# Performance work log

Hardware: AMD Instinct MI355X
Metric: run time of the kernel (lower is better)

The kernel has to match this reference:

```python
import jax, jax.numpy as jnp
import numpy as np

D_MODEL = 1024
NUM_HEADS = 16
HEAD_DIM = D_MODEL // NUM_HEADS
B, S = 4, 2048


def _xavier(key, shape, gain=0.1):
    fan_in, fan_out = shape[1], shape[0]
    a = gain * np.sqrt(6.0 / (fan_in + fan_out))
    return jax.random.uniform(key, shape, jnp.float32, -a, a)


def setup_inputs() -> dict:
    key = jax.random.key(0)
    ks = jax.random.split(key, 11)
    inp = {
        "q": jax.random.normal(ks[0], (B, S, D_MODEL), jnp.float32),
        "k": jax.random.normal(ks[1], (B, S, D_MODEL), jnp.float32),
        "v": jax.random.normal(ks[2], (B, S, D_MODEL), jnp.float32),
        # nn.Linear weights are [out, in]; y = x @ W.T + b
        "Wq": _xavier(ks[3], (D_MODEL, D_MODEL)),
        "bq": jnp.zeros((D_MODEL,), jnp.float32),
        "Wk": _xavier(ks[4], (D_MODEL, D_MODEL)),
        "bk": jnp.zeros((D_MODEL,), jnp.float32),
        "Wv": _xavier(ks[5], (D_MODEL, D_MODEL)),
        "bv": jnp.zeros((D_MODEL,), jnp.float32),
        "Wo": _xavier(ks[6], (D_MODEL, D_MODEL)),
        "bo": jnp.zeros((D_MODEL,), jnp.float32),
    }
    return inp


def reference(q, k, v, Wq, bq, Wk, bk, Wv, bv, Wo, bo):
    b = q.shape[0]
    qh = (q @ Wq.T + bq).reshape(b, -1, NUM_HEADS, HEAD_DIM).transpose(0, 2, 1, 3)
    kh = (k @ Wk.T + bk).reshape(b, -1, NUM_HEADS, HEAD_DIM).transpose(0, 2, 1, 3)
    vh = (v @ Wv.T + bv).reshape(b, -1, NUM_HEADS, HEAD_DIM).transpose(0, 2, 1, 3)
    # NOTE: original (buggy) module scales by sqrt(d_model), not sqrt(head_dim)
    scale = 1.0 / jnp.sqrt(jnp.float32(D_MODEL))
    scores = jnp.einsum('bhqd,bhkd->bhqk', qh, kh) * scale  # [B,H,S,S]
    attn = jax.nn.softmax(scores, axis=-1)
    out = jnp.einsum('bhqk,bhkd->bhqd', attn, vh)
    out = out.transpose(0, 2, 1, 3).reshape(b, -1, D_MODEL)
    return out @ Wo.T + bo
```

## Files before the change

### kernel.cpp

```cpp
#include <hip/hip_runtime.h>

typedef unsigned short u16;
typedef short bf16x8 __attribute__((ext_vector_type(8)));
typedef float f32x4 __attribute__((ext_vector_type(4)));
typedef u16 u16x8 __attribute__((ext_vector_type(8)));

__device__ __forceinline__ u16 f2bf(float f) {
  unsigned u = __float_as_uint(f);
  u = u + 0x7fffu + ((u >> 16) & 1u);
  return (u16)(u >> 16);
}

__device__ __forceinline__ float fexp2(float x) {
#if __has_builtin(__builtin_amdgcn_exp2f)
  return __builtin_amdgcn_exp2f(x);
#else
  return exp2f(x);
#endif
}

#define GLD16(ldsp, gp)                                                         \
  __builtin_amdgcn_global_load_lds(                                             \
      (__attribute__((address_space(1))) void*)(void*)(gp),                     \
      (__attribute__((address_space(3))) void*)(ldsp), 16, 0, 0)

#define CVTPK(dst, lo, hi)                                                      \
  asm("v_cvt_pk_bf16_f32 %0, %1, %2" : "=v"(dst) : "v"(lo), "v"(hi))
#define PACK8(dst, a0, a1, a2, a3, a4, a5, a6, a7)                              \
  do {                                                                          \
    union { unsigned u_[4]; bf16x8 v_; } c_;                                    \
    CVTPK(c_.u_[0], a0, a1); CVTPK(c_.u_[1], a2, a3);                           \
    CVTPK(c_.u_[2], a4, a5); CVTPK(c_.u_[3], a6, a7);                           \
    dst = c_.v_;                                                                \
  } while (0)

__global__ __launch_bounds__(256) void pack_w4(const float* __restrict__ w0,
                                               const float* __restrict__ w1,
                                               const float* __restrict__ w2,
                                               const float* __restrict__ w3,
                                               u16* __restrict__ out) {
  int i = blockIdx.x * 256 + threadIdx.x;
  int which = i >> 17;
  const float* src = which == 0 ? w0 : which == 1 ? w1 : which == 2 ? w2 : w3;
  int j = i & 131071;
  const float4* p = (const float4*)src + (size_t)j * 2;
  float4 a = p[0], b = p[1];
  u16x8 r;
  r[0] = f2bf(a.x); r[1] = f2bf(a.y); r[2] = f2bf(a.z); r[3] = f2bf(a.w);
  r[4] = f2bf(b.x); r[5] = f2bf(b.y); r[6] = f2bf(b.z); r[7] = f2bf(b.w);
  *(u16x8*)(out + (size_t)i * 8) = r;
}

__global__ __launch_bounds__(256, 4)
void gemm_qkv(const float* __restrict__ qi, const float* __restrict__ ki,
              const float* __restrict__ vi, const u16* __restrict__ wbf,
              const float* __restrict__ bq, const float* __restrict__ bk,
              const float* __restrict__ bv, u16* __restrict__ qo,
              u16* __restrict__ ko, u16* __restrict__ vo) {
  constexpr int K = 1024;
  __shared__ __align__(16) u16 As[128 * 64];
  __shared__ __align__(16) u16 Bs[128 * 64];
  const int z = blockIdx.z;
  const float* Af = z == 0 ? qi : z == 1 ? ki : vi;
  const u16* Bw = wbf + ((size_t)z << 20);
  const float* bias = z == 0 ? bq : z == 1 ? bk : bv;

  const int t = threadIdx.x;
  const int w = t >> 6, l = t & 63;
  const int lr = l & 15, lg = l >> 4;
  const int flat = blockIdx.x | (blockIdx.y << 3);
  const int swz = ((flat & 7) << 6) | (flat >> 3);
  const int row0 = (swz >> 3) * 128, col0 = (swz & 7) * 128;
  const int wm = (w >> 1) * 64, wn = (w & 1) * 64;

  f32x4 acc[4][4] = {};

  const int ar = t >> 3;
  const int xw = ((t & 7) ^ (ar & 7)) * 16;
  const float* gA = Af + (size_t)(row0 + ar) * K + (t & 7) * 8;
  const u16* gB = Bw + (size_t)(col0 + ar) * K + (((t & 7) ^ (ar & 7)) * 8);
  u16* lB = &Bs[w * 512];

  float4 a0[4], a1[4];
#pragma unroll
  for (int j = 0; j < 4; ++j) {
    const float* p = gA + (size_t)j * 32 * K;
    a0[j] = *(const float4*)p;
    a1[j] = *(const float4*)(p + 4);
  }

  for (int kt = 0; kt < 16; ++kt) {
#pragma unroll
    for (int j = 0; j < 4; ++j)
      GLD16(lB + j * 2048, gB + (size_t)j * 32 * K + kt * 64);
#pragma unroll
    for (int j = 0; j < 4; ++j) {
      bf16x8 c;
      PACK8(c, a0[j].x, a0[j].y, a0[j].z, a0[j].w, a1[j].x, a1[j].y, a1[j].z, a1[j].w);
      *(bf16x8*)((char*)As + (ar + j * 32) * 128 + xw) = c;
    }
    __syncthreads();
    if (kt < 15) {
#pragma unroll
      for (int j = 0; j < 4; ++j) {
        const float* p = gA + (size_t)j * 32 * K + (kt + 1) * 64;
        a0[j] = *(const float4*)p;
        a1[j] = *(const float4*)(p + 4);
      }
    }
#pragma unroll
    for (int kh2 = 0; kh2 < 2; ++kh2) {
      bf16x8 aF[4], bF[4];
      const int bc = (kh2 * 64 + lg * 16) ^ ((lr & 7) * 16);
#pragma unroll
      for (int mi = 0; mi < 4; ++mi)
        aF[mi] = *(const bf16x8*)((const char*)As + (wm + mi * 16 + lr) * 128 + bc);
#pragma unroll
      for (int ni = 0; ni < 4; ++ni)
        bF[ni] = *(const bf16x8*)((const char*)Bs + (wn + ni * 16 + lr) * 128 + bc);
#pragma unroll
      for (int mi = 0; mi < 4; ++mi)
#pragma unroll
        for (int ni = 0; ni < 4; ++ni)
          acc[mi][ni] = __builtin_amdgcn_mfma_f32_16x16x32_bf16(aF[mi], bF[ni],
                                                                acc[mi][ni], 0, 0, 0);
    }
    __syncthreads();
  }

#pragma unroll
  for (int mi = 0; mi < 4; ++mi) {
#pragma unroll
    for (int ni = 0; ni < 4; ++ni) {
      const int n = col0 + wn + ni * 16 + lr;
      const float bvv = bias[n];
#pragma unroll
      for (int r = 0; r < 4; ++r) {
        const int m = row0 + wm + mi * 16 + lg * 4 + r;
        const float vv = acc[mi][ni][r] + bvv;
        const int bI = m >> 11, s = m & 2047, h = n >> 6, d = n & 63;
        if (z == 0) {
          qo[((size_t)((bI << 4) + h) * 2048 + s) * 64 + d] = f2bf(vv * 0.045084223f);
        } else if (z == 1) {
          ko[((size_t)((bI << 4) + h) * 2048 + s) * 64 + d] = f2bf(vv);
        } else {
          int bh = (bI << 4) + h, tile = s >> 6, kp = s & 63;
          int kM = kp >> 5, k5 = kp & 31;
          int kpp = kM * 32 + ((k5 >> 2) & 3) * 8 + (k5 >> 4) * 4 + (k5 & 3);
          int chunk = (kpp >> 3) ^ (d & 7);
          vo[((size_t)bh << 17) + tile * 4096 + d * 64 + chunk * 8 + (kpp & 7)] = f2bf(vv);
        }
      }
    }
  }
}

__global__ __launch_bounds__(256, 3)
void gemm_out(const u16* __restrict__ A, const u16* __restrict__ B,
              const float* __restrict__ bias, float* __restrict__ outp) {
  constexpr int K = 1024;
  __shared__ __align__(16) u16 As[128 * 64];
  __shared__ __align__(16) u16 Bs[128 * 64];
  const int t = threadIdx.x;
  const int w = t >> 6;
  const int l = t & 63;
  const int lr = l & 15, lg = l >> 4;
  const int flat = blockIdx.x | (blockIdx.y << 3);
  const int swz = ((flat & 7) << 6) | (flat >> 3);
  const int row0 = (swz >> 3) * 128, col0 = (swz & 7) * 128;
  const int wm = (w >> 1) * 64, wn = (w & 1) * 64;

  f32x4 acc[4][4] = {};

  const int srow = t >> 3;
  const int scol = ((t & 7) ^ (srow & 7)) * 8;
  const u16* gA = A + (size_t)(row0 + srow) * K + scol;
  const u16* gB = B + (size_t)(col0 + srow) * K + scol;
  u16* lA = &As[w * 512];
  u16* lB = &Bs[w * 512];

  for (int k0 = 0; k0 < K; k0 += 64) {
#pragma unroll
    for (int j = 0; j < 4; ++j) {
      GLD16(lA + j * 2048, gA + (size_t)j * 32 * K + k0);
      GLD16(lB + j * 2048, gB + (size_t)j * 32 * K + k0);
    }
    __syncthreads();
#pragma unroll
    for (int kh2 = 0; kh2 < 2; ++kh2) {
      bf16x8 aF[4], bF[4];
      const int bc = (kh2 * 64 + lg * 16) ^ ((lr & 7) * 16);
#pragma unroll
      for (int mi = 0; mi < 4; ++mi)
        aF[mi] = *(const bf16x8*)((const char*)As + (wm + mi * 16 + lr) * 128 + bc);
#pragma unroll
      for (int ni = 0; ni < 4; ++ni)
        bF[ni] = *(const bf16x8*)((const char*)Bs + (wn + ni * 16 + lr) * 128 + bc);
#pragma unroll
      for (int mi = 0; mi < 4; ++mi)
#pragma unroll
        for (int ni = 0; ni < 4; ++ni)
          acc[mi][ni] = __builtin_amdgcn_mfma_f32_16x16x32_bf16(aF[mi], bF[ni],
                                                                acc[mi][ni], 0, 0, 0);
    }
    __syncthreads();
  }

#pragma unroll
  for (int mi = 0; mi < 4; ++mi)
#pragma unroll
    for (int ni = 0; ni < 4; ++ni) {
      const int n = col0 + wn + ni * 16 + lr;
      const float bv = bias[n];
#pragma unroll
      for (int r = 0; r < 4; ++r) {
        const int m = row0 + wm + mi * 16 + lg * 4 + r;
        outp[(size_t)m * 1024 + n] = acc[mi][ni][r] + bv;
      }
    }
}

__global__ __launch_bounds__(256, 4)
void attn_fwd(const u16* __restrict__ qh, const u16* __restrict__ kh,
              const u16* __restrict__ vp, u16* __restrict__ aout) {
  __shared__ __align__(16) u16 Ks[2][4096];
  __shared__ __align__(16) u16 Vl[2][4096];
  const int t = threadIdx.x;
  const int w = t >> 6, l = t & 63;
  const int lr = l & 15, lg = l >> 4;
  const int flat = blockIdx.x | (blockIdx.y << 4);
  const int swz = ((flat & 7) << 7) | (flat >> 3);
  const int qb = swz & 15, bh = swz >> 4;
  const int q0 = qb * 128 + w * 32;

  bf16x8 qf[2][2];
#pragma unroll
  for (int qi = 0; qi < 2; ++qi) {
    const u16* qp = qh + ((size_t)bh * 2048 + q0 + qi * 16 + lr) * 64 + lg * 8;
    qf[qi][0] = *(const bf16x8*)qp;
    qf[qi][1] = *(const bf16x8*)(qp + 32);
  }

  f32x4 o0[4] = {}, o1[4] = {};
  f32x4 sm0 = {}, sm1 = {};
  const bf16x8 ones = {16256, 16256, 16256, 16256, 16256, 16256, 16256, 16256};

  const int krow = t >> 3, kseg = t & 7;
  const u16* gK = kh + ((size_t)bh * 2048 + krow) * 64 + ((kseg ^ (krow & 7)) * 8);
  const u16* gV = vp + ((size_t)bh << 17) + t * 8;

  const int xo0 = (lg * 16) ^ ((lr & 7) * 16);
  const int xo1 = xo0 ^ 64;

  {
    u16* kd = &Ks[0][0] + w * 512;
    u16* vd = &Vl[0][0] + w * 512;
    GLD16(kd, gK); GLD16(kd + 2048, gK + 2048);
    GLD16(vd, gV); GLD16(vd + 2048, gV + 2048);
    gK += 4096; gV += 4096;
  }
  __syncthreads();

  for (int tix = 0; tix < 32; ++tix) {
    const int cur = tix & 1;
    if (tix < 31) {
      u16* kd = &Ks[cur ^ 1][0] + w * 512;
      u16* vd = &Vl[cur ^ 1][0] + w * 512;
      GLD16(kd, gK); GLD16(kd + 2048, gK + 2048);
      GLD16(vd, gV); GLD16(vd + 2048, gV + 2048);
      gK += 4096; gV += 4096;
    }
    const char* kb = (const char*)&Ks[cur][0];
    f32x4 s0[4], s1[4];
    __builtin_amdgcn_s_setprio(1);
#pragma unroll
    for (int cq = 0; cq < 4; ++cq) {
      const char* rowp = kb + (cq * 16 + lr) * 128;
      bf16x8 kf0 = *(const bf16x8*)(rowp + xo0);
      bf16x8 kf1 = *(const bf16x8*)(rowp + xo1);
      f32x4 a = {}, b2 = {};
      a  = __builtin_amdgcn_mfma_f32_16x16x32_bf16(kf0, qf[0][0], a, 0, 0, 0);
      a  = __builtin_amdgcn_mfma_f32_16x16x32_bf16(kf1, qf[0][1], a, 0, 0, 0);
      b2 = __builtin_amdgcn_mfma_f32_16x16x32_bf16(kf0, qf[1][0], b2, 0, 0, 0);
      b2 = __builtin_amdgcn_mfma_f32_16x16x32_bf16(kf1, qf[1][1], b2, 0, 0, 0);
      s0[cq] = a; s1[cq] = b2;
    }
    __builtin_amdgcn_s_setprio(0);
    float p0[16], p1[16];
#pragma unroll
    for (int cq = 0; cq < 4; ++cq)
#pragma unroll
      for (int r = 0; r < 4; ++r) {
        p0[cq * 4 + r] = fexp2(s0[cq][r]);
        p1[cq * 4 + r] = fexp2(s1[cq][r]);
      }
    bf16x8 pA0, pA1, pB0, pB1;
    PACK8(pA0, p0[0], p0[1], p0[2], p0[3], p0[4], p0[5], p0[6], p0[7]);
    PACK8(pA1, p0[8], p0[9], p0[10], p0[11], p0[12], p0[13], p0[14], p0[15]);
    PACK8(pB0, p1[0], p1[1], p1[2], p1[3], p1[4], p1[5], p1[6], p1[7]);
    PACK8(pB1, p1[8], p1[9], p1[10], p1[11], p1[12], p1[13], p1[14], p1[15]);
    __builtin_amdgcn_s_setprio(1);
    sm0 = __builtin_amdgcn_mfma_f32_16x16x32_bf16(pA0, ones, sm0, 0, 0, 0);
    sm0 = __builtin_amdgcn_mfma_f32_16x16x32_bf16(pA1, ones, sm0, 0, 0, 0);
    sm1 = __builtin_amdgcn_mfma_f32_16x16x32_bf16(pB0, ones, sm1, 0, 0, 0);
    sm1 = __builtin_amdgcn_mfma_f32_16x16x32_bf16(pB1, ones, sm1, 0, 0, 0);
    const char* vbb = (const char*)&Vl[cur][0];
#pragma unroll
    for (int dc = 0; dc < 4; ++dc) {
      const char* rp = vbb + (dc * 16 + lr) * 128;
      bf16x8 vA = *(const bf16x8*)(rp + xo0);
      bf16x8 vB = *(const bf16x8*)(rp + xo1);
      o0[dc] = __builtin_amdgcn_mfma_f32_16x16x32_bf16(pA0, vA, o0[dc], 0, 0, 0);
      o0[dc] = __builtin_amdgcn_mfma_f32_16x16x32_bf16(pA1, vB, o0[dc], 0, 0, 0);
      o1[dc] = __builtin_amdgcn_mfma_f32_16x16x32_bf16(pB0, vA, o1[dc], 0, 0, 0);
      o1[dc] = __builtin_amdgcn_mfma_f32_16x16x32_bf16(pB1, vB, o1[dc], 0, 0, 0);
    }
    __builtin_amdgcn_s_setprio(0);
    __syncthreads();
  }

  const int b = bh >> 4, h = bh & 15;
#pragma unroll
  for (int r = 0; r < 4; ++r) {
    const float dA = 1.f / sm0[r];
    const float dB = 1.f / sm1[r];
    const size_t rowA = (size_t)b * 2048 + q0 + lg * 4 + r;
#pragma unroll
    for (int dc = 0; dc < 4; ++dc) {
      aout[rowA * 1024 + h * 64 + dc * 16 + lr] = f2bf(o0[dc][r] * dA);
      aout[(rowA + 16) * 1024 + h * 64 + dc * 16 + lr] = f2bf(o1[dc][r] * dB);
    }
  }
}

extern "C" void kernel_launch(void* const* d_in, const int* in_sizes, int n_in,
                              void* d_out, int out_size, void* d_ws, size_t ws_size,
                              hipStream_t stream) {
  const float* q  = (const float*)d_in[0];
  const float* k  = (const float*)d_in[1];
  const float* v  = (const float*)d_in[2];
  const float* Wq = (const float*)d_in[3];
  const float* bq = (const float*)d_in[4];
  const float* Wk = (const float*)d_in[5];
  const float* bk = (const float*)d_in[6];
  const float* Wv = (const float*)d_in[7];
  const float* bv = (const float*)d_in[8];
  const float* Wo = (const float*)d_in[9];
  const float* bo = (const float*)d_in[10];

  char* ws = (char*)d_ws;
  u16* wbf  = (u16*)(ws);
  u16* aout = (u16*)(ws + (8ull << 20));
  u16* qhB  = (u16*)(ws + (24ull << 20));
  u16* khB  = (u16*)(ws + (40ull << 20));
  u16* vtB  = (u16*)(ws + (56ull << 20));

  pack_w4<<<2048, 256, 0, stream>>>(Wq, Wk, Wv, Wo, wbf);
  gemm_qkv<<<dim3(8, 64, 3), 256, 0, stream>>>(q, k, v, wbf, bq, bk, bv,
                                               qhB, khB, vtB);
  attn_fwd<<<dim3(16, 64), 256, 0, stream>>>(qhB, khB, vtB, aout);
  gemm_out<<<dim3(8, 64), 256, 0, stream>>>(aout, wbf + (3u << 20), bo,
                                            (float*)d_out);

  (void)in_sizes; (void)n_in; (void)out_size; (void)ws_size;
}
```

Before: 167.6 us.

## Software-pipeline QK^T one tile ahead of softmax/PV with triple-buffered V

Restructures the attention main loop so that the QK^T MFMAs for the next K tile are issued before the exp/pack/PV work of the current tile. V gets a three-slot ring buffer so V can be staged further ahead, and the loop is unrolled by two with alternating score registers. The goal is to overlap the exp (VALU/transcendental) work with matrix-core work and hide LDS latency. In exchange it uses more LDS and more registers, and launch bounds drop from 4 to 3 blocks per CU, which lowers occupancy.

New measurement: 172.7 us. 1.03x slower.

```diff
diff --git a/kernel.cpp b/kernel.cpp
--- a/kernel.cpp
+++ b/kernel.cpp
@@ -220,11 +220,73 @@
     }
 }
 
-__global__ __launch_bounds__(256, 4)
+#define QKC(KB, D0, D1)                                                         \
+  do {                                                                          \
+    const char* kb_ = (const char*)(KB);                                        \
+    _Pragma("unroll")                                                           \
+    for (int cq = 0; cq < 4; ++cq) {                                            \
+      const char* rowp_ = kb_ + (cq * 16 + lr) * 128;                           \
+      bf16x8 kf0_ = *(const bf16x8*)(rowp_ + xo0);                              \
+      bf16x8 kf1_ = *(const bf16x8*)(rowp_ + xo1);                              \
+      f32x4 a_ = {}, b_ = {};                                                   \
+      a_ = __builtin_amdgcn_mfma_f32_16x16x32_bf16(kf0_, qf[0][0], a_, 0, 0, 0);\
+      a_ = __builtin_amdgcn_mfma_f32_16x16x32_bf16(kf1_, qf[0][1], a_, 0, 0, 0);\
+      b_ = __builtin_amdgcn_mfma_f32_16x16x32_bf16(kf0_, qf[1][0], b_, 0, 0, 0);\
+      b_ = __builtin_amdgcn_mfma_f32_16x16x32_bf16(kf1_, qf[1][1], b_, 0, 0, 0);\
+      D0[cq] = a_; D1[cq] = b_;                                                 \
+    }                                                                           \
+  } while (0)
+
+#define STAGEKV(KSLOT)                                                          \
+  do {                                                                          \
+    u16* kd_ = &Ks[KSLOT][0] + w * 512;                                         \
+    u16* vd_ = &Vl[0][0] + vs * 4096 + w * 512;      \
+    GLD16(kd_, gK); GLD16(kd_ + 2048, gK + 2048);                               \
+    GLD16(vd_, gV); GLD16(vd_ + 2048, gV + 2048);                               \
+    gK += 4096; gV += 4096;                                                     \
+  } while (0)
+
+#define SOFTPV(SIN0, SIN1)                                                      \
+  do {                                                                          \
+    _Pragma("unroll")                                                           \
+    for (int cq = 0; cq < 4; ++cq) {                                            \
+      _Pragma("unroll")                                                         \
+      for (int r = 0; r < 4; ++r) {                                             \
+        SIN0[cq][r] = fexp2(SIN0[cq][r]);                                       \
+        SIN1[cq][r] = fexp2(SIN1[cq][r]);                                       \
+      }                                                                         \
+    }                                                                           \
+    bf16x8 pA0_, pA1_, pB0_, pB1_;                                              \
+    PACK8(pA0_, SIN0[0][0], SIN0[0][1], SIN0[0][2], SIN0[0][3],                 \
+                SIN0[1][0], SIN0[1][1], SIN0[1][2], SIN0[1][3]);                \
+    PACK8(pA1_, SIN0[2][0], SIN0[2][1], SIN0[2][2], SIN0[2][3],                 \
+                SIN0[3][0], SIN0[3][1], SIN0[3][2], SIN0[3][3]);                \
+    PACK8(pB0_, SIN1[0][0], SIN1[0][1], SIN1[0][2], SIN1[0][3],                 \
+                SIN1[1][0], SIN1[1][1], SIN1[1][2], SIN1[1][3]);                \
+    PACK8(pB1_, SIN1[2][0], SIN1[2][1], SIN1[2][2], SIN1[2][3],                 \
+                SIN1[3][0], SIN1[3][1], SIN1[3][2], SIN1[3][3]);                \
+    sm0 = __builtin_amdgcn_mfma_f32_16x16x32_bf16(pA0_, ones, sm0, 0, 0, 0);    \
+    sm0 = __builtin_amdgcn_mfma_f32_16x16x32_bf16(pA1_, ones, sm0, 0, 0, 0);    \
+    sm1 = __builtin_amdgcn_mfma_f32_16x16x32_bf16(pB0_, ones, sm1, 0, 0, 0);    \
+    sm1 = __builtin_amdgcn_mfma_f32_16x16x32_bf16(pB1_, ones, sm1, 0, 0, 0);    \
+    const char* vbb_ = (const char*)(&Vl[0][0] + vu * 4096);     \
+    _Pragma("unroll")                                                           \
+    for (int dc = 0; dc < 4; ++dc) {                                            \
+      const char* rp_ = vbb_ + (dc * 16 + lr) * 128;                            \
+      bf16x8 vA_ = *(const bf16x8*)(rp_ + xo0);                                 \
+      bf16x8 vB_ = *(const bf16x8*)(rp_ + xo1);                                 \
+      o0[dc] = __builtin_amdgcn_mfma_f32_16x16x32_bf16(pA0_, vA_, o0[dc], 0,0,0);\
+      o0[dc] = __builtin_amdgcn_mfma_f32_16x16x32_bf16(pA1_, vB_, o0[dc], 0,0,0);\
+      o1[dc] = __builtin_amdgcn_mfma_f32_16x16x32_bf16(pB0_, vA_, o1[dc], 0,0,0);\
+      o1[dc] = __builtin_amdgcn_mfma_f32_16x16x32_bf16(pB1_, vB_, o1[dc], 0,0,0);\
+    }                                                                           \
+  } while (0)
+
+__global__ __launch_bounds__(256, 3)
 void attn_fwd(const u16* __restrict__ qh, const u16* __restrict__ kh,
               const u16* __restrict__ vp, u16* __restrict__ aout) {
   __shared__ __align__(16) u16 Ks[2][4096];
-  __shared__ __align__(16) u16 Vl[2][4096];
+  __shared__ __align__(16) u16 Vl[3][4096];
   const int t = threadIdx.x;
   const int w = t >> 6, l = t & 63;
   const int lr = l & 15, lg = l >> 4;
@@ -252,71 +314,31 @@
   const int xo0 = (lg * 16) ^ ((lr & 7) * 16);
   const int xo1 = xo0 ^ 64;
 
-  {
-    u16* kd = &Ks[0][0] + w * 512;
-    u16* vd = &Vl[0][0] + w * 512;
-    GLD16(kd, gK); GLD16(kd + 2048, gK + 2048);
-    GLD16(vd, gV); GLD16(vd + 2048, gV + 2048);
-    gK += 4096; gV += 4096;
-  }
+  f32x4 sA0[4], sA1[4], sB0[4], sB1[4];
+  int vu = 0, vs = 0;
+
+  STAGEKV(0);
   __syncthreads();
-
-  for (int tix = 0; tix < 32; ++tix) {
-    const int cur = tix & 1;
-    if (tix < 31) {
-      u16* kd = &Ks[cur ^ 1][0] + w * 512;
-      u16* vd = &Vl[cur ^ 1][0] + w * 512;
-      GLD16(kd, gK); GLD16(kd + 2048, gK + 2048);
-      GLD16(vd, gV); GLD16(vd + 2048, gV + 2048);
-      gK += 4096; gV += 4096;
-    }
-    const char* kb = (const char*)&Ks[cur][0];
-    f32x4 s0[4], s1[4];
-    __builtin_amdgcn_s_setprio(1);
-#pragma unroll
-    for (int cq = 0; cq < 4; ++cq) {
-      const char* rowp = kb + (cq * 16 + lr) * 128;
-      bf16x8 kf0 = *(const bf16x8*)(rowp + xo0);
-      bf16x8 kf1 = *(const bf16x8*)(rowp + xo1);
-      f32x4 a = {}, b2 = {};
-      a  = __builtin_amdgcn_mfma_f32_16x16x32_bf16(kf0, qf[0][0], a, 0, 0, 0);
-      a  = __builtin_amdgcn_mfma_f32_16x16x32_bf16(kf1, qf[0][1], a, 0, 0, 0);
-      b2 = __builtin_amdgcn_mfma_f32_16x16x32_bf16(kf0, qf[1][0], b2, 0, 0, 0);
-      b2 = __builtin_amdgcn_mfma_f32_16x16x32_bf16(kf1, qf[1][1], b2, 0, 0, 0);
-      s0[cq] = a; s1[cq] = b2;
-    }
-    __builtin_amdgcn_s_setprio(0);
-    float p0[16], p1[16];
-#pragma unroll
-    for (int cq = 0; cq < 4; ++cq)
-#pragma unroll
-      for (int r = 0; r < 4; ++r) {
-        p0[cq * 4 + r] = fexp2(s0[cq][r]);
-        p1[cq * 4 + r] = fexp2(s1[cq][r]);
-      }
-    bf16x8 pA0, pA1, pB0, pB1;
-    PACK8(pA0, p0[0], p0[1], p0[2], p0[3], p0[4], p0[5], p0[6], p0[7]);
-    PACK8(pA1, p0[8], p0[9], p0[10], p0[11], p0[12], p0[13], p0[14], p0[15]);
-    PACK8(pB0, p1[0], p1[1], p1[2], p1[3], p1[4], p1[5], p1[6], p1[7]);
-    PACK8(pB1, p1[8], p1[9], p1[10], p1[11], p1[12], p1[13], p1[14], p1[15]);
-    __builtin_amdgcn_s_setprio(1);
-    sm0 = __builtin_amdgcn_mfma_f32_16x16x32_bf16(pA0, ones, sm0, 0, 0, 0);
-    sm0 = __builtin_amdgcn_mfma_f32_16x16x32_bf16(pA1, ones, sm0, 0, 0, 0);
-    sm1 = __builtin_amdgcn_mfma_f32_16x16x32_bf16(pB0, ones, sm1, 0, 0, 0);
-    sm1 = __builtin_amdgcn_mfma_f32_16x16x32_bf16(pB1, ones, sm1, 0, 0, 0);
-    const char* vbb = (const char*)&Vl[cur][0];
-#pragma unroll
-    for (int dc = 0; dc < 4; ++dc) {
-      const char* rp = vbb + (dc * 16 + lr) * 128;
-      bf16x8 vA = *(const bf16x8*)(rp + xo0);
-      bf16x8 vB = *(const bf16x8*)(rp + xo1);
-      o0[dc] = __builtin_amdgcn_mfma_f32_16x16x32_bf16(pA0, vA, o0[dc], 0, 0, 0);
-      o0[dc] = __builtin_amdgcn_mfma_f32_16x16x32_bf16(pA1, vB, o0[dc], 0, 0, 0);
-      o1[dc] = __builtin_amdgcn_mfma_f32_16x16x32_bf16(pB0, vA, o1[dc], 0, 0, 0);
-      o1[dc] = __builtin_amdgcn_mfma_f32_16x16x32_bf16(pB1, vB, o1[dc], 0, 0, 0);
-    }
-    __builtin_amdgcn_s_setprio(0);
-    __syncthreads();
+  vs = 1;
+  STAGEKV(1);
+  QKC(&Ks[0][0], sA0, sA1);
+  __syncthreads();
+  vs = 2;
+
+  for (int T = 0; T < 32; T += 2) {
+    if (T < 30) STAGEKV(0);
+    QKC(&Ks[1][0], sB0, sB1);
+    SOFTPV(sA0, sA1);
+    __syncthreads();
+    vu = (vu == 2) ? 0 : vu + 1;
+    vs = (vs == 2) ? 0 : vs + 1;
+
+    if (T < 30) STAGEKV(1);
+    if (T < 30) QKC(&Ks[0][0], sA0, sA1);
+    SOFTPV(sB0, sB1);
+    __syncthreads();
+    vu = (vu == 2) ? 0 : vu + 1;
+    vs = (vs == 2) ? 0 : vs + 1;
   }
 
   const int b = bh >> 4, h = bh & 15;
```
